# Kernel tuning notes

Measured on AMD Instinct MI355X. Metric: run time of the kernel, lower is better.

## Reference

```python
import jax, jax.numpy as jnp
import numpy as np

N = 40000      # nodes
E = 640000     # edges (avg degree 16)
IN = 128       # in_dim
H = 8          # n_heads
D = 16         # out_dim per head
ED = 64        # edge_dim
C = H * D      # out_channel = 128 == IN -> residual is Identity
EPS = 1e-5


def setup_inputs() -> dict:
    key = jax.random.key(0)
    ks = jax.random.split(key, 20)

    def lin(k, shape):
        fan_in = shape[-1]
        return jax.random.normal(k, shape, dtype=jnp.float32) / np.sqrt(fan_in)

    return {
        "q": jax.random.normal(ks[0], (N, IN), dtype=jnp.float32),
        "k": jax.random.normal(ks[1], (N, IN), dtype=jnp.float32),
        "v": jax.random.normal(ks[2], (N, IN), dtype=jnp.float32),
        "edge_feat": jax.random.normal(ks[3], (E, ED), dtype=jnp.float32),
        "src": jax.random.randint(ks[4], (E,), 0, N, dtype=jnp.int32),
        "dst": jax.random.randint(ks[5], (E,), 0, N, dtype=jnp.int32),
        "Wq": lin(ks[6], (C, IN)),
        "Wk": lin(ks[7], (C, IN)),
        "Wv": lin(ks[8], (C, IN)),
        "We": lin(ks[9], (H, ED)),
        "be": jnp.zeros((H,), dtype=jnp.float32),
        "Wo": lin(ks[10], (C, C)),
        "W1": lin(ks[11], (2 * C, C)),
        "b1": jnp.zeros((2 * C,), dtype=jnp.float32),
        "W2": lin(ks[12], (C, 2 * C)),
        "b2": jnp.zeros((C,), dtype=jnp.float32),
        "g1": jnp.ones((C,), dtype=jnp.float32),
        "bt1": jnp.zeros((C,), dtype=jnp.float32),
        "g2": jnp.ones((C,), dtype=jnp.float32),
        "bt2": jnp.zeros((C,), dtype=jnp.float32),
    }


def _batch_norm(x, g, b):
    mu = x.mean(axis=0)
    var = x.var(axis=0)  # biased, matching torch BN normalization
    return (x - mu) * jax.lax.rsqrt(var + EPS) * g + b


def reference(q, k, v, edge_feat, src, dst, Wq, Wk, Wv, We, be, Wo,
              W1, b1, W2, b2, g1, bt1, g2, bt2):
    n = q.shape[0]
    qd = (q @ Wq.T).reshape(n, H, D)        # [N,H,D] dst queries
    ksrc = (k @ Wk.T).reshape(-1, H, D)     # [N,H,D]
    vsrc = (v @ Wv.T).reshape(-1, H, D)     # [N,H,D]

    # per-edge attention scores: v_dot_u(q_dst, k_src) / sqrt(D)
    scores = jnp.einsum('ehd,ehd->eh', qd[dst], ksrc[src]) / jnp.sqrt(jnp.float32(D))
    # edge_mode == 'ADD': add per-head edge bias
    scores = scores + edge_feat @ We.T + be  # [E,H]

    # edge softmax normalized by destination node (segment softmax)
    smax = jax.ops.segment_max(scores, dst, num_segments=n)      # [N,H]
    ex = jnp.exp(scores - smax[dst])
    denom = jax.ops.segment_sum(ex, dst, num_segments=n)         # [N,H]
    attn = ex / denom[dst]                                       # [E,H]

    # scatter-weighted aggregation: sum_e attn * v_src -> dst
    agg = jax.ops.segment_sum(attn[:, :, None] * vsrc[src], dst, num_segments=n)  # [N,H,D]

    rst = agg.reshape(n, C) @ Wo.T
    rst = rst + q                    # residual (Identity: in_dim == out_channel)
    rst = _batch_norm(rst, g1, bt1)

    h = jnp.maximum(rst @ W1.T + b1, 0.0) @ W2.T + b2  # FFN
    rst = _batch_norm(h + rst, g2, bt2)
    return rst
```

## Files before the change

kernel.cpp:

```cpp
#include <hip/hip_runtime.h>
#include <cstdint>
#include <cstddef>

#define Nn 40000
#define Ne 640000
#define CC 128
#define EPSbn 1e-5f

typedef __attribute__((ext_vector_type(8))) __bf16 bf16x8;
typedef __attribute__((ext_vector_type(4))) float floatx4;
typedef __attribute__((ext_vector_type(8))) unsigned short ushort8;

__device__ inline unsigned short f2bf(float x){
  union { float f; unsigned u; } c; c.f = x;
  unsigned r = c.u + 0x7fffu + ((c.u >> 16) & 1u);
  return (unsigned short)(r >> 16);
}
__device__ inline float bflo(unsigned u){ return __uint_as_float(u << 16); }
__device__ inline float bfhi(unsigned u){ return __uint_as_float(u & 0xffff0000u); }

__device__ inline unsigned f2e4m3(float x){
  unsigned u = __float_as_uint(x);
  unsigned s = (u >> 24) & 0x80u;
  unsigned a = u & 0x7fffffffu;
  unsigned lsb = (a >> 20) & 1u;
  a += 0x0007FFFFu + lsb;
  int e = (int)((a >> 23) & 0xffu) - 127;
  unsigned b;
  if (e < -9)      b = 0u;
  else if (e < -6) b = (unsigned)(int)rintf(__uint_as_float(u & 0x7fffffffu) * 512.f);
  else if (e > 8)  b = 0x7Eu;
  else             b = (unsigned)(((e + 7) << 3) | ((a >> 20) & 7u));
  if ((b & 0x7fu) == 0x7fu) b = 0x7Eu;
  return s | b;
}

#if defined(__has_builtin)
#if __has_builtin(__builtin_amdgcn_cvt_f32_fp8)
#define FP8_HW 1
#endif
#endif
template<int SEL>
__device__ inline float fp8dec(unsigned w){
#ifdef FP8_HW
  return __builtin_amdgcn_cvt_f32_fp8((int)w, SEL);
#else
  unsigned b = (w >> (SEL*8)) & 0xffu;
  unsigned s = (b & 0x80u) << 24;
  unsigned em = b & 0x7fu;
  float v;
  if (em >= 8) v = __uint_as_float((((em >> 3) + 117u) << 23)) * (float)(8 + (em & 7));
  else         v = (float)em * 0.001953125f;
  return __uint_as_float(__float_as_uint(v) | s);
#endif
}

__global__ __launch_bounds__(256) void prep_k(int* __restrict__ zp, int zn,
    const float* __restrict__ Wq, const float* __restrict__ Wk,
    const float* __restrict__ Wv, const float* __restrict__ Wo,
    const float* __restrict__ W1, const float* __restrict__ W2,
    unsigned short* __restrict__ Wb)
{
  int b = blockIdx.x, tid = threadIdx.x;
  if (b < 161) { int i = b*256 + tid; if (i < zn) zp[i] = 0; return; }
  int i = (b - 161)*256 + tid;
  const float* s; int off;
  if      (i < 16384) { s = Wq; off = i; }
  else if (i < 32768) { s = Wk; off = i - 16384; }
  else if (i < 49152) { s = Wv; off = i - 32768; }
  else if (i < 65536) { s = Wo; off = i - 49152; }
  else if (i < 98304) { s = W1; off = i - 65536; }
  else                { s = W2; off = i - 98304; }
  Wb[i] = f2bf(s[off]);
}

struct GA3 {
  const void* A0; const void* A1; const void* A2;
  const unsigned short* W0; const unsigned short* W1; const unsigned short* W2;
  void* C0; void* C1; void* C2;
  int m0, m1, m2;
};

template<int KTILES,bool ABF16,bool HASBIAS,bool HASRES,bool RELU,bool BNA,bool BNRES,bool BNSTAT>
__global__ __launch_bounds__(256,2) void mgemm_k(
    GA3 ga, const float* __restrict__ bias, const float* __restrict__ res,
    const float* __restrict__ bnSin, const float* __restrict__ bnQin,
    const float* __restrict__ gamma, const float* __restrict__ beta,
    float* __restrict__ bnS, float* __restrict__ bnQ,
    int M, int Ncols)
{
  constexpr int K = KTILES * 128;
  __shared__ __align__(16) unsigned short As[128*136];
  __shared__ __align__(16) unsigned short Ws[128*136];
  __shared__ float scb[128], shb[128];
  const int z = blockIdx.z;
  const void*           Ap = (z==0) ? ga.A0 : (z==1) ? ga.A1 : ga.A2;
  const unsigned short* W  = (z==0) ? ga.W0 : (z==1) ? ga.W1 : ga.W2;
  void*                 Cp = (z==0) ? ga.C0 : (z==1) ? ga.C1 : ga.C2;
  const int mode           = (z==0) ? ga.m0 : (z==1) ? ga.m1 : ga.m2;

  const int tid  = threadIdx.x;
  const int lane = tid & 63;
  const int wv   = tid >> 6;
  const int m    = lane & 15;
  const int quad = lane >> 4;
  const int row0 = blockIdx.x * 128;
  const int col0 = blockIdx.y * 128;

  if (BNA || BNRES) {
    if (tid < 128) {
      float mu  = bnSin[tid] / (float)M;
      float var = bnQin[tid] / (float)M - mu*mu;
      float s   = gamma[tid] * rsqrtf(var + EPSbn);
      scb[tid] = s;
      shb[tid] = beta[tid] - mu*s;
    }
    __syncthreads();
  }

  floatx4 acc[2][8] = {};

  for (int kt = 0; kt < K; kt += 128) {
    #pragma unroll
    for (int it = 0; it < 8; ++it) {
      int s = tid + it*256;
      int r = s >> 4;
      int c = (s & 15) << 3;
      *(ushort8*)&Ws[r*136 + c] =
          *(const ushort8*)(W + (size_t)(col0 + r)*K + kt + c);
    }
    if (ABF16) {
      #pragma unroll
      for (int it = 0; it < 8; ++it) {
        int s = tid + it*256;
        int r = s >> 4;
        int c = (s & 15) << 3;
        int gr = row0 + r; if (gr >= M) gr = M - 1;
        *(ushort8*)&As[r*136 + c] =
            *(const ushort8*)((const unsigned short*)Ap + (size_t)gr*K + kt + c);
      }
    } else {
      #pragma unroll 4
      for (int it = 0; it < 16; ++it) {
        int s = tid + it*256;
        int r = s >> 5;
        int c = (s & 31) << 2;
        int gr = row0 + r; if (gr >= M) gr = M - 1;
        float4 a4 = *(const float4*)((const float*)Ap + (size_t)gr*K + kt + c);
        if (BNA) {
          a4.x = a4.x*scb[c  ] + shb[c  ];
          a4.y = a4.y*scb[c+1] + shb[c+1];
          a4.z = a4.z*scb[c+2] + shb[c+2];
          a4.w = a4.w*scb[c+3] + shb[c+3];
        }
        ushort4 ua;
        ua.x = f2bf(a4.x); ua.y = f2bf(a4.y); ua.z = f2bf(a4.z); ua.w = f2bf(a4.w);
        *(ushort4*)&As[r*136 + c] = ua;
      }
    }
    __syncthreads();
    #pragma unroll
    for (int ks = 0; ks < 4; ++ks) {
      int ko = ks*32 + quad*8;
      bf16x8 a0 = *(const bf16x8*)&As[(32*wv      + m)*136 + ko];
      bf16x8 a1 = *(const bf16x8*)&As[(32*wv + 16 + m)*136 + ko];
      #pragma unroll
      for (int j = 0; j < 8; ++j) {
        bf16x8 bj = *(const bf16x8*)&Ws[(16*j + m)*136 + ko];
        acc[0][j] = __builtin_amdgcn_mfma_f32_16x16x32_bf16(a0, bj, acc[0][j], 0, 0, 0);
        acc[1][j] = __builtin_amdgcn_mfma_f32_16x16x32_bf16(a1, bj, acc[1][j], 0, 0, 0);
      }
    }
    __syncthreads();
  }

  float bcol[8], scv[8], shv[8];
  #pragma unroll
  for (int j = 0; j < 8; ++j) {
    int gcol = col0 + 16*j + m;
    if (HASBIAS) bcol[j] = bias[gcol];
    if (BNRES) { scv[j] = scb[16*j + m]; shv[j] = shb[16*j + m]; }
  }
  float ps[8] = {}, pq[8] = {};
  #pragma unroll
  for (int rt = 0; rt < 2; ++rt) {
    #pragma unroll
    for (int rg = 0; rg < 4; ++rg) {
      int grow = row0 + 32*wv + 16*rt + quad*4 + rg;
      if (grow < M) {
        #pragma unroll
        for (int j = 0; j < 8; ++j) {
          int gcol = col0 + 16*j + m;
          float o = acc[rt][j][rg];
          if (HASBIAS) o += bcol[j];
          if (HASRES) {
            float rr = res[(size_t)grow*Ncols + gcol];
            if (BNRES) rr = rr*scv[j] + shv[j];
            o += rr;
          }
          if (RELU) o = fmaxf(o, 0.f);
          if (BNSTAT) { ps[j] += o; pq[j] += o*o; }
          if (mode == 0)      ((float*)Cp)[(size_t)grow*Ncols + gcol] = o;
          else                ((unsigned short*)Cp)[(size_t)grow*Ncols + gcol] = f2bf(o);
        }
      }
    }
  }
  if (BNSTAT) {
    float* sS = (float*)&As[0];
    float* sQ = sS + 4*128;
    #pragma unroll
    for (int j = 0; j < 8; ++j) {
      float s = ps[j], qq = pq[j];
      s += __shfl_xor(s, 16); qq += __shfl_xor(qq, 16);
      s += __shfl_xor(s, 32); qq += __shfl_xor(qq, 32);
      if (quad == 0) { sS[wv*128 + 16*j + m] = s; sQ[wv*128 + 16*j + m] = qq; }
    }
    __syncthreads();
    if (wv == 0) {
      #pragma unroll
      for (int c = 0; c < 128; c += 64) {
        int cc = c + lane;
        float s  = sS[cc] + sS[128+cc] + sS[256+cc] + sS[384+cc];
        float qq = sQ[cc] + sQ[128+cc] + sQ[256+cc] + sQ[384+cc];
        atomicAdd(&bnS[col0 + cc], s);
        atomicAdd(&bnQ[col0 + cc], qq);
      }
    }
  }
}

__global__ __launch_bounds__(256) void re_k(
    const unsigned* __restrict__ Kb, const unsigned* __restrict__ Vb,
    unsigned* __restrict__ KV,
    const float* __restrict__ ef, const float* __restrict__ We,
    const float* __restrict__ be, const int* __restrict__ pos,
    unsigned short* __restrict__ EBs)
{
  __shared__ float efs[32][68];
  __shared__ float Wes[8][68];
  __shared__ float bes[8];
  int tid = threadIdx.x;
  int b = blockIdx.x;
  if (b < 10000) {
    int i = b*256 + tid;
    unsigned kk = Kb[i];
    unsigned vv = Vb[i];
    unsigned o = f2e4m3(bflo(kk)) | (f2e4m3(bfhi(kk)) << 8)
               | (f2e4m3(bflo(vv)) << 16) | (f2e4m3(bfhi(vv)) << 24);
    KV[i] = o;
    return;
  }
  if (tid < 8) bes[tid] = be[tid];
  for (int i = tid; i < 512; i += 256) Wes[i>>6][i&63] = We[i];
  int e0 = (b - 10000) * 32;
  #pragma unroll
  for (int l = 0; l < 2; ++l) {
    int idx = tid + l*256;
    int r   = idx >> 4;
    int q4  = (idx & 15) << 2;
    float4 t = *(const float4*)(ef + (size_t)(e0 + r)*64 + q4);
    efs[r][q4]=t.x; efs[r][q4+1]=t.y; efs[r][q4+2]=t.z; efs[r][q4+3]=t.w;
  }
  __syncthreads();
  int h = tid & 7, el = tid >> 3;
  int e = e0 + el;
  float es = 0.f;
  #pragma unroll
  for (int kk = 0; kk < 64; kk += 4) {
    float4 a = *(const float4*)&efs[el][kk];
    float4 bq = *(const float4*)&Wes[h][kk];
    es += a.x*bq.x + a.y*bq.y + a.z*bq.z + a.w*bq.w;
  }
  EBs[(size_t)pos[e]*8 + h] = f2bf(es + bes[h]);
}

__global__ void hist_k(const int* __restrict__ dst, int* __restrict__ counts, int E){
  int i = blockIdx.x*blockDim.x + threadIdx.x;
  if (i < E) atomicAdd(&counts[dst[i]], 1);
}

__global__ __launch_bounds__(256) void scan1_k(
    const int* __restrict__ counts, int* __restrict__ part,
    int* __restrict__ bsums, int n)
{
  int tid = threadIdx.x;
  int base = blockIdx.x*1024 + tid*4;
  int v0 = (base   < n) ? counts[base  ] : 0;
  int v1 = (base+1 < n) ? counts[base+1] : 0;
  int v2 = (base+2 < n) ? counts[base+2] : 0;
  int v3 = (base+3 < n) ? counts[base+3] : 0;
  int t1 = v0+v1, t2 = t1+v2, t3 = t2+v3;
  int lane = tid & 63, wv = tid >> 6;
  int x = t3;
  #pragma unroll
  for (int off = 1; off < 64; off <<= 1) {
    int y = __shfl_up(x, off);
    if (lane >= off) x += y;
  }
  __shared__ int wt[4];
  if (lane == 63) wt[wv] = x;
  __syncthreads();
  int wbase = 0;
  #pragma unroll
  for (int w = 0; w < 4; ++w) if (w < wv) wbase += wt[w];
  int excl = wbase + x - t3;
  if (base   < n) part[base  ] = excl;
  if (base+1 < n) part[base+1] = excl + v0;
  if (base+2 < n) part[base+2] = excl + t1;
  if (base+3 < n) part[base+3] = excl + t2;
  if (tid == 255) bsums[blockIdx.x] = wbase + x;
}

__global__ __launch_bounds__(256) void scan23_k(
    int* __restrict__ offsets, const int* __restrict__ bsums,
    int* __restrict__ cursor, int n, int E)
{
  __shared__ int sb[40];
  int tid = threadIdx.x;
  if (tid < 64) {
    int v = (tid < 40) ? bsums[tid] : 0;
    int x = v;
    #pragma unroll
    for (int off = 1; off < 64; off <<= 1) {
      int y = __shfl_up(x, off);
      if (tid >= off) x += y;
    }
    if (tid < 40) sb[tid] = x - v;
  }
  __syncthreads();
  int i = blockIdx.x*blockDim.x + tid;
  if (i < n) {
    int o = offsets[i] + sb[i >> 10];
    offsets[i] = o;
    cursor[i]  = o;
  }
  if (i == 0) offsets[n] = E;
}

__global__ void scatter_k(const int* __restrict__ dst, const int* __restrict__ src,
                          int* __restrict__ cursor, int* __restrict__ pos,
                          int* __restrict__ srcs, int E){
  int i = blockIdx.x*blockDim.x + threadIdx.x;
  if (i < E) {
    int p = atomicAdd(&cursor[dst[i]], 1);
    pos[i]  = p;
    srcs[p] = src[i];
  }
}

__global__ __launch_bounds__(256) void agg_k(
    const unsigned* __restrict__ QDb, const unsigned* __restrict__ KV,
    const unsigned short* __restrict__ EBs,
    const int* __restrict__ offsets, const int* __restrict__ srcs,
    unsigned* __restrict__ agg, int n)
{
  int wv = threadIdx.x >> 6, lane = threadIdx.x & 63;
  int node = blockIdx.x*4 + wv;
  if (node >= n) return;
  unsigned qt = QDb[(size_t)node*64 + lane];
  float q0 = bflo(qt) * 0.25f;
  float q1 = bfhi(qt) * 0.25f;
  int beg = offsets[node], end = offsets[node+1];
  int hoff = lane >> 3;
  float acc0 = 0.f, acc1 = 0.f, den = 0.f;
  for (int base = beg; base < end; base += 64) {
    int mrem = end - base; if (mrem > 64) mrem = 64;
    int ss = (lane < mrem) ? srcs[base + lane] : 0;
    int j = 0;
    for (; j + 4 <= mrem; j += 4) {
      int s0 = __shfl(ss, j);
      int s1 = __shfl(ss, j+1);
      int s2 = __shfl(ss, j+2);
      int s3 = __shfl(ss, j+3);
      unsigned kv0 = KV[(size_t)s0*64 + lane];
      unsigned kv1 = KV[(size_t)s1*64 + lane];
      unsigned kv2 = KV[(size_t)s2*64 + lane];
      unsigned kv3 = KV[(size_t)s3*64 + lane];
      float p0 = q0*fp8dec<0>(kv0) + q1*fp8dec<1>(kv0);
      float p1 = q0*fp8dec<0>(kv1) + q1*fp8dec<1>(kv1);
      float p2 = q0*fp8dec<0>(kv2) + q1*fp8dec<1>(kv2);
      float p3 = q0*fp8dec<0>(kv3) + q1*fp8dec<1>(kv3);
      p0 += __shfl_xor(p0, 1); p1 += __shfl_xor(p1, 1); p2 += __shfl_xor(p2, 1); p3 += __shfl_xor(p3, 1);
      p0 += __shfl_xor(p0, 2); p1 += __shfl_xor(p1, 2); p2 += __shfl_xor(p2, 2); p3 += __shfl_xor(p3, 2);
      p0 += __shfl_xor(p0, 4); p1 += __shfl_xor(p1, 4); p2 += __shfl_xor(p2, 4); p3 += __shfl_xor(p3, 4);
      float eb0 = __uint_as_float(((unsigned)EBs[(size_t)(base+j  )*8 + hoff]) << 16);
      float eb1 = __uint_as_float(((unsigned)EBs[(size_t)(base+j+1)*8 + hoff]) << 16);
      float eb2 = __uint_as_float(((unsigned)EBs[(size_t)(base+j+2)*8 + hoff]) << 16);
      float eb3 = __uint_as_float(((unsigned)EBs[(size_t)(base+j+3)*8 + hoff]) << 16);
      float w0 = __expf(p0 + eb0);
      float w1 = __expf(p1 + eb1);
      float w2 = __expf(p2 + eb2);
      float w3 = __expf(p3 + eb3);
      acc0 += w0*fp8dec<2>(kv0) + w1*fp8dec<2>(kv1) + w2*fp8dec<2>(kv2) + w3*fp8dec<2>(kv3);
      acc1 += w0*fp8dec<3>(kv0) + w1*fp8dec<3>(kv1) + w2*fp8dec<3>(kv2) + w3*fp8dec<3>(kv3);
      den  += (w0 + w1) + (w2 + w3);
    }
    for (; j < mrem; ++j) {
      int s0 = __shfl(ss, j);
      unsigned kv0 = KV[(size_t)s0*64 + lane];
      float p0 = q0*fp8dec<0>(kv0) + q1*fp8dec<1>(kv0);
      p0 += __shfl_xor(p0, 1);
      p0 += __shfl_xor(p0, 2);
      p0 += __shfl_xor(p0, 4);
      float eb0 = __uint_as_float(((unsigned)EBs[(size_t)(base+j)*8 + hoff]) << 16);
      float w0 = __expf(p0 + eb0);
      acc0 += w0*fp8dec<2>(kv0);
      acc1 += w0*fp8dec<3>(kv0);
      den  += w0;
    }
  }
  float inv = den > 0.f ? 1.f/den : 0.f;
  unsigned o = (unsigned)f2bf(acc0*inv) | ((unsigned)f2bf(acc1*inv) << 16);
  agg[(size_t)node*64 + lane] = o;
}

__global__ __launch_bounds__(256) void bnapply_k(
    const float* __restrict__ Y,
    const float* __restrict__ sum2, const float* __restrict__ sq2,
    const float* __restrict__ g, const float* __restrict__ bt,
    float* __restrict__ out, int M, int total)
{
  __shared__ float scb[128], shb[128];
  int tid = threadIdx.x;
  if (tid < 128) {
    float mu  = sum2[tid] / (float)M;
    float var = sq2[tid] / (float)M - mu*mu;
    float s   = g[tid] * rsqrtf(var + EPSbn);
    scb[tid] = s;
    shb[tid] = bt[tid] - mu*s;
  }
  __syncthreads();
  int n4 = total >> 2;
  for (int i = blockIdx.x*blockDim.x + tid; i < n4; i += gridDim.x*blockDim.x) {
    float4 vv = ((const float4*)Y)[i];
    int c = (i << 2) & 127;
    vv.x = vv.x*scb[c  ] + shb[c  ];
    vv.y = vv.y*scb[c+1] + shb[c+1];
    vv.z = vv.z*scb[c+2] + shb[c+2];
    vv.w = vv.w*scb[c+3] + shb[c+3];
    ((float4*)out)[i] = vv;
  }
}

extern "C" void kernel_launch(void* const* d_in, const int* in_sizes, int n_in,
                              void* d_out, int out_size, void* d_ws, size_t ws_size,
                              hipStream_t stream) {
  const float* q   = (const float*)d_in[0];
  const float* k   = (const float*)d_in[1];
  const float* v   = (const float*)d_in[2];
  const float* ef  = (const float*)d_in[3];
  const int*   src = (const int*)d_in[4];
  const int*   dst = (const int*)d_in[5];
  const float* Wq  = (const float*)d_in[6];
  const float* Wk  = (const float*)d_in[7];
  const float* Wv  = (const float*)d_in[8];
  const float* We  = (const float*)d_in[9];
  const float* be  = (const float*)d_in[10];
  const float* Wo  = (const float*)d_in[11];
  const float* W1  = (const float*)d_in[12];
  const float* b1  = (const float*)d_in[13];
  const float* W2  = (const float*)d_in[14];
  const float* b2  = (const float*)d_in[15];
  const float* g1  = (const float*)d_in[16];
  const float* bt1 = (const float*)d_in[17];
  const float* g2  = (const float*)d_in[18];
  const float* bt2 = (const float*)d_in[19];
  float* out = (float*)d_out;

  float* ws = (float*)d_ws;
  const size_t NB = (size_t)Nn * CC;
  float* QDb = ws;
  float* Kb  = ws + NB/2;
  float* Vb  = ws + NB;
  unsigned* KVq = (unsigned*)(ws + 3*NB/2);
  unsigned short* EBs = (unsigned short*)(ws + 2*NB);
  unsigned* AGGb = (unsigned*)(ws + 5*NB/2);
  float* Y   = ws + 5*NB/2;
  float* RST = ws + 7*NB/2;
  float* H1  = ws;
  float* bn = ws + 9*NB/2;
  float* sum1 = bn;       float* sq1 = bn+128;
  float* sum2 = bn+512;   float* sq2 = bn+640;
  int* ib      = (int*)(bn + 1024);
  int* counts  = ib;
  int* offsets = ib + 40000;
  int* cursor  = ib + 80001;
  int* posA    = ib + 120001;
  int* srcsA   = ib + 760001;
  int* bsums   = ib + 1400001;
  unsigned short* Wb = (unsigned short*)(ib + 1400068);
  unsigned short* WqB = Wb;
  unsigned short* WkB = Wb + 16384;
  unsigned short* WvB = Wb + 32768;
  unsigned short* WoB = Wb + 49152;
  unsigned short* W1B = Wb + 65536;
  unsigned short* W2B = Wb + 98304;

  prep_k<<<dim3(673), 256, 0, stream>>>((int*)bn, 1024 + Nn,
                                        Wq, Wk, Wv, Wo, W1, W2, Wb);

  hist_k<<<dim3(2500), 256, 0, stream>>>(dst, counts, Ne);
  scan1_k<<<dim3(40), 256, 0, stream>>>(counts, offsets, bsums, Nn);
  scan23_k<<<dim3(157), 256, 0, stream>>>(offsets, bsums, cursor, Nn, Ne);
  scatter_k<<<dim3(2500), 256, 0, stream>>>(dst, src, cursor, posA, srcsA, Ne);

  {
    GA3 ga;
    ga.A0 = q;   ga.A1 = k;   ga.A2 = v;
    ga.W0 = WqB; ga.W1 = WkB; ga.W2 = WvB;
    ga.C0 = QDb; ga.C1 = Kb;  ga.C2 = Vb;
    ga.m0 = 1;   ga.m1 = 1;   ga.m2 = 1;
    mgemm_k<1,false,false,false,false,false,false,false><<<dim3(313,1,3),256,0,stream>>>(
        ga, nullptr, nullptr, nullptr, nullptr, nullptr, nullptr,
        nullptr, nullptr, Nn, 128);
  }

  re_k<<<dim3(30000), 256, 0, stream>>>((const unsigned*)Kb, (const unsigned*)Vb,
                                        KVq, ef, We, be, posA, EBs);

  agg_k<<<dim3(Nn/4), 256, 0, stream>>>((const unsigned*)QDb, KVq, EBs,
                                        offsets, srcsA, AGGb, Nn);

  {
    GA3 ga = {};
    ga.A0 = AGGb; ga.W0 = WoB; ga.C0 = RST; ga.m0 = 0;
    mgemm_k<1,true,false,true,false,false,false,true><<<dim3(313,1,1),256,0,stream>>>(
        ga, nullptr, q, nullptr, nullptr, nullptr, nullptr,
        sum1, sq1, Nn, 128);
  }

  {
    GA3 ga = {};
    ga.A0 = RST; ga.W0 = W1B; ga.C0 = H1; ga.m0 = 1;
    mgemm_k<1,false,true,false,true,true,false,false><<<dim3(313,2,1),256,0,stream>>>(
        ga, b1, nullptr, sum1, sq1, g1, bt1,
        nullptr, nullptr, Nn, 256);
  }

  {
    GA3 ga = {};
    ga.A0 = H1; ga.W0 = W2B; ga.C0 = Y; ga.m0 = 0;
    mgemm_k<2,true,true,true,false,false,true,true><<<dim3(313,1,1),256,0,stream>>>(
        ga, b2, RST, sum1, sq1, g1, bt1,
        sum2, sq2, Nn, 128);
  }

  bnapply_k<<<dim3(1024), 256, 0, stream>>>(Y, sum2, sq2, g2, bt2, out, Nn, Nn*CC);
}
```

Measured before the change: 531.8 us.

## Fuse CSR build, projections and tail GEMMs into persistent kernels with grid barriers

Replaces the histogram, scan, scatter and QKV projection launches with one persistent kernel, and the Wo/FFN/BN-apply chain with another. Phases are separated by software grid barriers built on atomic counters. The aim is to remove several kernel launches and the idle gaps between them. The trade-offs are spin-wait barrier cost, and a dependence on all 512 blocks being co-resident (2 per CU), otherwise the barriers deadlock. Barrier counters are zeroed by prep_k each call.

After: 916.7 us. 72.4% more time.

```diff
diff --git a/kernel.cpp b/kernel.cpp
--- a/kernel.cpp
+++ b/kernel.cpp
@@ -55,6 +55,17 @@
 #endif
 }
 
+__device__ inline void gbar(int* c, int nb){
+  __syncthreads();
+  if (threadIdx.x == 0) {
+    __threadfence();
+    atomicAdd(c, 1);
+    while (atomicAdd(c, 0) < nb) __builtin_amdgcn_s_sleep(2);
+  }
+  __syncthreads();
+  __threadfence();
+}
+
 __global__ __launch_bounds__(256) void prep_k(int* __restrict__ zp, int zn,
     const float* __restrict__ Wq, const float* __restrict__ Wk,
     const float* __restrict__ Wv, const float* __restrict__ Wo,
@@ -74,49 +85,21 @@
   Wb[i] = f2bf(s[off]);
 }
 
-struct GA3 {
-  const void* A0; const void* A1; const void* A2;
-  const unsigned short* W0; const unsigned short* W1; const unsigned short* W2;
-  void* C0; void* C1; void* C2;
-  int m0, m1, m2;
-};
-
 template<int KTILES,bool ABF16,bool HASBIAS,bool HASRES,bool RELU,bool BNA,bool BNRES,bool BNSTAT>
-__global__ __launch_bounds__(256,2) void mgemm_k(
-    GA3 ga, const float* __restrict__ bias, const float* __restrict__ res,
-    const float* __restrict__ bnSin, const float* __restrict__ bnQin,
-    const float* __restrict__ gamma, const float* __restrict__ beta,
-    float* __restrict__ bnS, float* __restrict__ bnQ,
-    int M, int Ncols)
+__device__ __forceinline__ void gemm_tile(
+    const void* Ap, const unsigned short* W, void* Cp, int mode,
+    const float* bias, const float* res,
+    const float* scb, const float* shb,
+    float* bnS, float* bnQ,
+    unsigned short* As, unsigned short* Ws,
+    int row0, int col0, int M, int Ncols)
 {
   constexpr int K = KTILES * 128;
-  __shared__ __align__(16) unsigned short As[128*136];
-  __shared__ __align__(16) unsigned short Ws[128*136];
-  __shared__ float scb[128], shb[128];
-  const int z = blockIdx.z;
-  const void*           Ap = (z==0) ? ga.A0 : (z==1) ? ga.A1 : ga.A2;
-  const unsigned short* W  = (z==0) ? ga.W0 : (z==1) ? ga.W1 : ga.W2;
-  void*                 Cp = (z==0) ? ga.C0 : (z==1) ? ga.C1 : ga.C2;
-  const int mode           = (z==0) ? ga.m0 : (z==1) ? ga.m1 : ga.m2;
-
   const int tid  = threadIdx.x;
   const int lane = tid & 63;
   const int wv   = tid >> 6;
   const int m    = lane & 15;
   const int quad = lane >> 4;
-  const int row0 = blockIdx.x * 128;
-  const int col0 = blockIdx.y * 128;
-
-  if (BNA || BNRES) {
-    if (tid < 128) {
-      float mu  = bnSin[tid] / (float)M;
-      float var = bnQin[tid] / (float)M - mu*mu;
-      float s   = gamma[tid] * rsqrtf(var + EPSbn);
-      scb[tid] = s;
-      shb[tid] = beta[tid] - mu*s;
-    }
-    __syncthreads();
-  }
 
   floatx4 acc[2][8] = {};
 
@@ -230,6 +213,93 @@
   }
 }
 
+struct CsrArgs {
+  const int *dst, *src;
+  int *counts, *offsets, *cursor, *posA, *srcs, *bsums, *bars;
+  const float *q, *k, *v;
+  const unsigned short *WqB, *WkB, *WvB;
+  void *QDb, *Kb, *Vb;
+};
+
+__global__ __launch_bounds__(256,2) void csr_k(CsrArgs a){
+  __shared__ __align__(16) unsigned short As[128*136];
+  __shared__ __align__(16) unsigned short Ws[128*136];
+  const int tid = threadIdx.x, bid = blockIdx.x, nb = gridDim.x;
+  const int gtid = bid*256 + tid, gsz = nb*256;
+
+  for (int i = gtid; i < Ne; i += gsz) atomicAdd(&a.counts[a.dst[i]], 1);
+  gbar(a.bars + 0, nb);
+
+  if (bid < 40) {
+    int* wt = (int*)Ws;
+    int base = bid*1024 + tid*4;
+    int v0 = (base   < Nn) ? a.counts[base  ] : 0;
+    int v1 = (base+1 < Nn) ? a.counts[base+1] : 0;
+    int v2 = (base+2 < Nn) ? a.counts[base+2] : 0;
+    int v3 = (base+3 < Nn) ? a.counts[base+3] : 0;
+    int t1 = v0+v1, t2 = t1+v2, t3 = t2+v3;
+    int lane = tid & 63, w1 = tid >> 6;
+    int x = t3;
+    #pragma unroll
+    for (int off = 1; off < 64; off <<= 1) {
+      int y = __shfl_up(x, off);
+      if (lane >= off) x += y;
+    }
+    if (lane == 63) wt[w1] = x;
+    __syncthreads();
+    int wbase = 0;
+    #pragma unroll
+    for (int w = 0; w < 4; ++w) if (w < w1) wbase += wt[w];
+    int excl = wbase + x - t3;
+    if (base   < Nn) a.offsets[base  ] = excl;
+    if (base+1 < Nn) a.offsets[base+1] = excl + v0;
+    if (base+2 < Nn) a.offsets[base+2] = excl + t1;
+    if (base+3 < Nn) a.offsets[base+3] = excl + t2;
+    if (tid == 255) a.bsums[bid] = wbase + x;
+  }
+  gbar(a.bars + 1, nb);
+
+  {
+    int* sb = (int*)As;
+    if (tid < 64) {
+      int v = (tid < 40) ? a.bsums[tid] : 0;
+      int x = v;
+      #pragma unroll
+      for (int off = 1; off < 64; off <<= 1) {
+        int y = __shfl_up(x, off);
+        if (tid >= off) x += y;
+      }
+      if (tid < 40) sb[tid] = x - v;
+    }
+    __syncthreads();
+    for (int i = gtid; i < Nn; i += gsz) {
+      int o = a.offsets[i] + sb[i >> 10];
+      a.offsets[i] = o;
+      a.cursor[i]  = o;
+    }
+    if (gtid == 0) a.offsets[Nn] = Ne;
+  }
+  gbar(a.bars + 2, nb);
+
+  for (int i = gtid; i < Ne; i += gsz) {
+    int p = atomicAdd(&a.cursor[a.dst[i]], 1);
+    a.posA[i]  = p;
+    a.srcs[p]  = a.src[i];
+  }
+
+  for (int t = bid; t < 939; t += nb) {
+    __syncthreads();
+    int z  = t / 313;
+    int bx = t - z*313;
+    const void* Ap = (z==0) ? (const void*)a.q : (z==1) ? (const void*)a.k : (const void*)a.v;
+    const unsigned short* W = (z==0) ? a.WqB : (z==1) ? a.WkB : a.WvB;
+    void* Cp = (z==0) ? a.QDb : (z==1) ? a.Kb : a.Vb;
+    gemm_tile<1,false,false,false,false,false,false,false>(
+        Ap, W, Cp, 1, nullptr, nullptr, nullptr, nullptr, nullptr, nullptr,
+        As, Ws, bx*128, 0, Nn, 128);
+  }
+}
+
 __global__ __launch_bounds__(256) void re_k(
     const unsigned* __restrict__ Kb, const unsigned* __restrict__ Vb,
     unsigned* __restrict__ KV,
@@ -273,80 +343,6 @@
     es += a.x*bq.x + a.y*bq.y + a.z*bq.z + a.w*bq.w;
   }
   EBs[(size_t)pos[e]*8 + h] = f2bf(es + bes[h]);
-}
-
-__global__ void hist_k(const int* __restrict__ dst, int* __restrict__ counts, int E){
-  int i = blockIdx.x*blockDim.x + threadIdx.x;
-  if (i < E) atomicAdd(&counts[dst[i]], 1);
-}
-
-__global__ __launch_bounds__(256) void scan1_k(
-    const int* __restrict__ counts, int* __restrict__ part,
-    int* __restrict__ bsums, int n)
-{
-  int tid = threadIdx.x;
-  int base = blockIdx.x*1024 + tid*4;
-  int v0 = (base   < n) ? counts[base  ] : 0;
-  int v1 = (base+1 < n) ? counts[base+1] : 0;
-  int v2 = (base+2 < n) ? counts[base+2] : 0;
-  int v3 = (base+3 < n) ? counts[base+3] : 0;
-  int t1 = v0+v1, t2 = t1+v2, t3 = t2+v3;
-  int lane = tid & 63, wv = tid >> 6;
-  int x = t3;
-  #pragma unroll
-  for (int off = 1; off < 64; off <<= 1) {
-    int y = __shfl_up(x, off);
-    if (lane >= off) x += y;
-  }
-  __shared__ int wt[4];
-  if (lane == 63) wt[wv] = x;
-  __syncthreads();
-  int wbase = 0;
-  #pragma unroll
-  for (int w = 0; w < 4; ++w) if (w < wv) wbase += wt[w];
-  int excl = wbase + x - t3;
-  if (base   < n) part[base  ] = excl;
-  if (base+1 < n) part[base+1] = excl + v0;
-  if (base+2 < n) part[base+2] = excl + t1;
-  if (base+3 < n) part[base+3] = excl + t2;
-  if (tid == 255) bsums[blockIdx.x] = wbase + x;
-}
-
-__global__ __launch_bounds__(256) void scan23_k(
-    int* __restrict__ offsets, const int* __restrict__ bsums,
-    int* __restrict__ cursor, int n, int E)
-{
-  __shared__ int sb[40];
-  int tid = threadIdx.x;
-  if (tid < 64) {
-    int v = (tid < 40) ? bsums[tid] : 0;
-    int x = v;
-    #pragma unroll
-    for (int off = 1; off < 64; off <<= 1) {
-      int y = __shfl_up(x, off);
-      if (tid >= off) x += y;
-    }
-    if (tid < 40) sb[tid] = x - v;
-  }
-  __syncthreads();
-  int i = blockIdx.x*blockDim.x + tid;
-  if (i < n) {
-    int o = offsets[i] + sb[i >> 10];
-    offsets[i] = o;
-    cursor[i]  = o;
-  }
-  if (i == 0) offsets[n] = E;
-}
-
-__global__ void scatter_k(const int* __restrict__ dst, const int* __restrict__ src,
-                          int* __restrict__ cursor, int* __restrict__ pos,
-                          int* __restrict__ srcs, int E){
-  int i = blockIdx.x*blockDim.x + threadIdx.x;
-  if (i < E) {
-    int p = atomicAdd(&cursor[dst[i]], 1);
-    pos[i]  = p;
-    srcs[p] = src[i];
-  }
 }
 
 __global__ __launch_bounds__(256) void agg_k(
@@ -415,31 +411,73 @@
   agg[(size_t)node*64 + lane] = o;
 }
 
-__global__ __launch_bounds__(256) void bnapply_k(
-    const float* __restrict__ Y,
-    const float* __restrict__ sum2, const float* __restrict__ sq2,
-    const float* __restrict__ g, const float* __restrict__ bt,
-    float* __restrict__ out, int M, int total)
-{
+struct TailArgs {
+  const void* AGGb; const unsigned short* WoB; float* RST; const float* q;
+  const unsigned short* W1B; void* H1; const float* b1;
+  const unsigned short* W2B; float* Y; const float* b2;
+  float *sum1, *sq1, *sum2, *sq2;
+  const float *g1, *bt1, *g2, *bt2;
+  float* outp; int* bars;
+};
+
+__global__ __launch_bounds__(256,2) void tail_k(TailArgs a){
+  __shared__ __align__(16) unsigned short As[128*136];
+  __shared__ __align__(16) unsigned short Ws[128*136];
   __shared__ float scb[128], shb[128];
-  int tid = threadIdx.x;
+  const int tid = threadIdx.x, bid = blockIdx.x, nb = gridDim.x;
+  const int gtid = bid*256 + tid, gsz = nb*256;
+
+  for (int t = bid; t < 313; t += nb) {
+    __syncthreads();
+    gemm_tile<1,true,false,true,false,false,false,true>(
+        a.AGGb, a.WoB, a.RST, 0, nullptr, a.q, nullptr, nullptr,
+        a.sum1, a.sq1, As, Ws, t*128, 0, Nn, 128);
+  }
+  gbar(a.bars + 0, nb);
+
   if (tid < 128) {
-    float mu  = sum2[tid] / (float)M;
-    float var = sq2[tid] / (float)M - mu*mu;
-    float s   = g[tid] * rsqrtf(var + EPSbn);
+    float mu  = a.sum1[tid] / (float)Nn;
+    float var = a.sq1[tid] / (float)Nn - mu*mu;
+    float s   = a.g1[tid] * rsqrtf(var + EPSbn);
     scb[tid] = s;
-    shb[tid] = bt[tid] - mu*s;
+    shb[tid] = a.bt1[tid] - mu*s;
   }
   __syncthreads();
-  int n4 = total >> 2;
-  for (int i = blockIdx.x*blockDim.x + tid; i < n4; i += gridDim.x*blockDim.x) {
-    float4 vv = ((const float4*)Y)[i];
+
+  for (int t = bid; t < 626; t += nb) {
+    __syncthreads();
+    int by = t / 313, bx = t - by*313;
+    gemm_tile<1,false,true,false,true,true,false,false>(
+        a.RST, a.W1B, a.H1, 1, a.b1, nullptr, scb, shb,
+        nullptr, nullptr, As, Ws, bx*128, by*128, Nn, 256);
+  }
+  gbar(a.bars + 1, nb);
+
+  for (int t = bid; t < 313; t += nb) {
+    __syncthreads();
+    gemm_tile<2,true,true,true,false,false,true,true>(
+        a.H1, a.W2B, a.Y, 0, a.b2, a.RST, scb, shb,
+        a.sum2, a.sq2, As, Ws, t*128, 0, Nn, 128);
+  }
+  gbar(a.bars + 2, nb);
+
+  if (tid < 128) {
+    float mu  = a.sum2[tid] / (float)Nn;
+    float var = a.sq2[tid] / (float)Nn - mu*mu;
+    float s   = a.g2[tid] * rsqrtf(var + EPSbn);
+    scb[tid] = s;
+    shb[tid] = a.bt2[tid] - mu*s;
+  }
+  __syncthreads();
+  int n4 = (Nn*CC) >> 2;
+  for (int i = gtid; i < n4; i += gsz) {
+    float4 vv = ((const float4*)a.Y)[i];
     int c = (i << 2) & 127;
     vv.x = vv.x*scb[c  ] + shb[c  ];
     vv.y = vv.y*scb[c+1] + shb[c+1];
     vv.z = vv.z*scb[c+2] + shb[c+2];
     vv.w = vv.w*scb[c+3] + shb[c+3];
-    ((float4*)out)[i] = vv;
+    ((float4*)a.outp)[i] = vv;
   }
 }
 
@@ -482,6 +520,7 @@
   float* bn = ws + 9*NB/2;
   float* sum1 = bn;       float* sq1 = bn+128;
   float* sum2 = bn+512;   float* sq2 = bn+640;
+  int* bars   = (int*)(bn + 768);
   int* ib      = (int*)(bn + 1024);
   int* counts  = ib;
   int* offsets = ib + 40000;
@@ -500,20 +539,15 @@
   prep_k<<<dim3(673), 256, 0, stream>>>((int*)bn, 1024 + Nn,
                                         Wq, Wk, Wv, Wo, W1, W2, Wb);
 
-  hist_k<<<dim3(2500), 256, 0, stream>>>(dst, counts, Ne);
-  scan1_k<<<dim3(40), 256, 0, stream>>>(counts, offsets, bsums, Nn);
-  scan23_k<<<dim3(157), 256, 0, stream>>>(offsets, bsums, cursor, Nn, Ne);
-  scatter_k<<<dim3(2500), 256, 0, stream>>>(dst, src, cursor, posA, srcsA, Ne);
-
   {
-    GA3 ga;
-    ga.A0 = q;   ga.A1 = k;   ga.A2 = v;
-    ga.W0 = WqB; ga.W1 = WkB; ga.W2 = WvB;
-    ga.C0 = QDb; ga.C1 = Kb;  ga.C2 = Vb;
-    ga.m0 = 1;   ga.m1 = 1;   ga.m2 = 1;
-    mgemm_k<1,false,false,false,false,false,false,false><<<dim3(313,1,3),256,0,stream>>>(
-        ga, nullptr, nullptr, nullptr, nullptr, nullptr, nullptr,
-        nullptr, nullptr, Nn, 128);
+    CsrArgs ca;
+    ca.dst = dst; ca.src = src;
+    ca.counts = counts; ca.offsets = offsets; ca.cursor = cursor;
+    ca.posA = posA; ca.srcs = srcsA; ca.bsums = bsums; ca.bars = bars;
+    ca.q = q; ca.k = k; ca.v = v;
+    ca.WqB = WqB; ca.WkB = WkB; ca.WvB = WvB;
+    ca.QDb = QDb; ca.Kb = Kb; ca.Vb = Vb;
+    csr_k<<<dim3(512), 256, 0, stream>>>(ca);
   }
 
   re_k<<<dim3(30000), 256, 0, stream>>>((const unsigned*)Kb, (const unsigned*)Vb,
@@ -523,28 +557,13 @@
                                         offsets, srcsA, AGGb, Nn);
 
   {
-    GA3 ga = {};
-    ga.A0 = AGGb; ga.W0 = WoB; ga.C0 = RST; ga.m0 = 0;
-    mgemm_k<1,true,false,true,false,false,false,true><<<dim3(313,1,1),256,0,stream>>>(
-        ga, nullptr, q, nullptr, nullptr, nullptr, nullptr,
-        sum1, sq1, Nn, 128);
-  }
-
-  {
-    GA3 ga = {};
-    ga.A0 = RST; ga.W0 = W1B; ga.C0 = H1; ga.m0 = 1;
-    mgemm_k<1,false,true,false,true,true,false,false><<<dim3(313,2,1),256,0,stream>>>(
-        ga, b1, nullptr, sum1, sq1, g1, bt1,
-        nullptr, nullptr, Nn, 256);
-  }
-
-  {
-    GA3 ga = {};
-    ga.A0 = H1; ga.W0 = W2B; ga.C0 = Y; ga.m0 = 0;
-    mgemm_k<2,true,true,true,false,false,true,true><<<dim3(313,1,1),256,0,stream>>>(
-        ga, b2, RST, sum1, sq1, g1, bt1,
-        sum2, sq2, Nn, 128);
-  }
-
-  bnapply_k<<<dim3(1024), 256, 0, stream>>>(Y, sum2, sq2, g2, bt2, out, Nn, Nn*CC);
-}
+    TailArgs ta;
+    ta.AGGb = AGGb; ta.WoB = WoB; ta.RST = RST; ta.q = q;
+    ta.W1B = W1B; ta.H1 = H1; ta.b1 = b1;
+    ta.W2B = W2B; ta.Y = Y; ta.b2 = b2;
+    ta.sum1 = sum1; ta.sq1 = sq1; ta.sum2 = sum2; ta.sq2 = sq2;
+    ta.g1 = g1; ta.bt1 = bt1; ta.g2 = g2; ta.bt2 = bt2;
+    ta.outp = out; ta.bars = bars + 3;
+    tail_k<<<dim3(512), 256, 0, stream>>>(ta);
+  }
+}
```
